# Kernel tuning notes

Measured on AMD Instinct MI355X. Metric: run time of the kernel, lower is better.

Reference implementation:

```python
import jax, jax.numpy as jnp
import numpy as np

NUM_HEADS = 16


def setup_inputs() -> dict:
    key = jax.random.key(0)
    k1, k2, k3, k4 = jax.random.split(key, 4)
    in_dim, out_dim = 1024, 1024
    x = jax.random.normal(k1, (4, 2048, in_dim), dtype=jnp.float32)
    # nn.Linear weights stored as [out, in]; we keep that convention.
    s = 1.0 / np.sqrt(in_dim)
    Wq = jax.random.uniform(k2, (out_dim, in_dim), jnp.float32, -s, s)
    Wk = jax.random.uniform(k3, (out_dim, in_dim), jnp.float32, -s, s)
    Wv = jax.random.uniform(k4, (out_dim, in_dim), jnp.float32, -s, s)
    return {"x": x, "Wq": Wq, "Wk": Wk, "Wv": Wv}


def reference(x, Wq, Wk, Wv):
    b, n, _ = x.shape
    out_dim = Wq.shape[0]
    h = NUM_HEADS
    d = out_dim // h  # head_dim

    def split_heads(t):  # [b,n,out] -> [b,h,n,d]
        return t.reshape(b, n, h, d).transpose(0, 2, 1, 3)

    q = split_heads(x @ Wq.T)
    k = split_heads(x @ Wk.T)
    v = split_heads(x @ Wv.T)

    scores = jnp.einsum("bhqd,bhkd->bhqk", q, k) / jnp.sqrt(jnp.float32(d))
    causal = jnp.tril(jnp.ones((n, n), dtype=bool))
    scores = jnp.where(causal, scores, -jnp.inf)
    attn = jax.nn.softmax(scores, axis=-1)
    out = jnp.einsum("bhqk,bhkd->bhqd", attn, v)
    return out.transpose(0, 2, 1, 3).reshape(b, n, out_dim)
```

## Files before the change

### kernel.cpp

```cpp
#include <hip/hip_runtime.h>

typedef __attribute__((ext_vector_type(8))) short short8;
typedef __attribute__((ext_vector_type(4))) short short4v;
typedef __attribute__((ext_vector_type(4))) float floatx4;
typedef __attribute__((ext_vector_type(16))) float floatx16;
typedef __attribute__((ext_vector_type(2))) int iv2;

#define GLOBAL_AS __attribute__((address_space(1)))
#define LDS_AS __attribute__((address_space(3)))

__device__ __forceinline__ short f2bs(float f) {
    union { float f; unsigned u; } v; v.f = f;
    unsigned r = v.u + 0x7fffu + ((v.u >> 16) & 1u);
    return (short)(r >> 16);
}

#if __has_builtin(__builtin_amdgcn_cvt_pk_bf16_f32)
typedef __attribute__((ext_vector_type(2))) __bf16 bf16x2;
__device__ __forceinline__ unsigned pk2(float a, float b) {
    union { bf16x2 v; unsigned u; } u;
    u.v = __builtin_amdgcn_cvt_pk_bf16_f32(a, b);
    return u.u;
}
#else
__device__ __forceinline__ unsigned pk2(float a, float b) {
    union { float f; unsigned u; } x, y; x.f = a; y.f = b;
    return ((y.u + 0x8000u) & 0xffff0000u) | ((x.u + 0x8000u) >> 16);
}
#endif

__global__ __launch_bounds__(256) void cast_all(const float* __restrict__ x,
                                                const float* __restrict__ Wq,
                                                const float* __restrict__ Wk,
                                                const float* __restrict__ Wv,
                                                short* __restrict__ xb,
                                                short* __restrict__ wb) {
    int b = blockIdx.x;
    int t = threadIdx.x;
    const float* src;
    short* dst;
    int idx;
    if (b < 8192) {
        src = x; dst = xb; idx = b * 1024 + t * 4;
    } else {
        int r = b - 8192;
        int wz = r >> 10;
        src = (wz == 0) ? Wq : (wz == 1) ? Wk : Wv;
        dst = wb + wz * (1 << 20);
        idx = (r & 1023) * 1024 + t * 4;
    }
    float4 v = *(const float4*)(src + idx);
    short4v o;
    o.x = f2bs(v.x); o.y = f2bs(v.y); o.z = f2bs(v.z); o.w = f2bs(v.w);
    *(short4v*)(dst + idx) = o;
}

__global__ __launch_bounds__(256) void qkv_gemm(const short* __restrict__ xb,
                                                const short* __restrict__ wb,
                                                short* __restrict__ qout,
                                                short* __restrict__ kout,
                                                short* __restrict__ vtout) {
    __shared__ short As[2][128 * 64];
    __shared__ short Bs[2][128 * 64];
    const int K = 1024;
    int tid = threadIdx.x;
    int lane = tid & 63;
    int wid = tid >> 6;
    int quad = lane >> 4;
    int l16 = lane & 15;
    int wm = (wid >> 1) * 64;
    int wn = (wid & 1) * 64;
    int bm = blockIdx.x * 128;
    int bn = blockIdx.y * 128;
    const short* W = wb + (size_t)blockIdx.z * K * 1024;

    floatx4 acc[4][4];
#pragma unroll
    for (int i = 0; i < 4; i++)
#pragma unroll
        for (int j = 0; j < 4; j++) acc[i][j] = (floatx4){0.f, 0.f, 0.f, 0.f};

    int srow = tid >> 3;
    int ssw = ((tid & 7) ^ (srow & 7)) * 8;

#define STAGE_AB(cb, kk) do { \
    _Pragma("unroll") for (int l = 0; l < 4; l++) { \
        const short* g = xb + (size_t)(bm + srow + l * 32) * K + (kk) + ssw; \
        __builtin_amdgcn_global_load_lds((const GLOBAL_AS void*)g, \
            (LDS_AS void*)(&As[cb][0] + tid * 8 + l * 2048), 16, 0, 0); \
    } \
    _Pragma("unroll") for (int l = 0; l < 4; l++) { \
        const short* g = W + (size_t)(bn + srow + l * 32) * K + (kk) + ssw; \
        __builtin_amdgcn_global_load_lds((const GLOBAL_AS void*)g, \
            (LDS_AS void*)(&Bs[cb][0] + tid * 8 + l * 2048), 16, 0, 0); \
    } \
} while (0)

    STAGE_AB(0, 0);

    for (int T = 0; T < 16; T++) {
        int cur = T & 1;
        __builtin_amdgcn_sched_barrier(0);
        __builtin_amdgcn_s_barrier();
        __builtin_amdgcn_sched_barrier(0);
        if (T < 15) {
            STAGE_AB(cur ^ 1, (T + 1) * 64);
            asm volatile("s_waitcnt vmcnt(8)" ::: "memory");
        } else {
            asm volatile("s_waitcnt vmcnt(0)" ::: "memory");
        }
        __builtin_amdgcn_sched_barrier(0);
        __builtin_amdgcn_s_barrier();
        __builtin_amdgcn_sched_barrier(0);

        const short* Ac = &As[cur][0];
        const short* Bc = &Bs[cur][0];
#pragma unroll
        for (int s = 0; s < 2; s++) {
            int slot = ((s * 4 + quad) ^ (l16 & 7)) * 8;
            short8 af[4], bf[4];
#pragma unroll
            for (int i = 0; i < 4; i++)
                af[i] = *(const short8*)(Ac + (wm + i * 16 + l16) * 64 + slot);
#pragma unroll
            for (int j = 0; j < 4; j++)
                bf[j] = *(const short8*)(Bc + (wn + j * 16 + l16) * 64 + slot);
#pragma unroll
            for (int i = 0; i < 4; i++)
#pragma unroll
                for (int j = 0; j < 4; j++)
                    acc[i][j] = __builtin_amdgcn_mfma_f32_16x16x32_bf16(af[i], bf[j], acc[i][j], 0, 0, 0);
        }
    }
#undef STAGE_AB

    if (blockIdx.z == 2) {
#pragma unroll
        for (int i = 0; i < 4; i++) {
#pragma unroll
            for (int j = 0; j < 4; j++) {
                int m = bm + wm + i * 16 + quad * 4;
                int c = bn + wn + j * 16 + l16;
                int b = m >> 11, nn = m & 2047, h = c >> 6, dd = c & 63;
                short4v pk;
                pk.x = f2bs(acc[i][j][0]);
                pk.y = f2bs(acc[i][j][1]);
                pk.z = f2bs(acc[i][j][2]);
                pk.w = f2bs(acc[i][j][3]);
                *(short4v*)(vtout + ((size_t)(b * 16 + h) * 64 + dd) * 2048 + nn) = pk;
            }
        }
    } else {
        short* dst = (blockIdx.z == 0) ? qout : kout;
        float qs = (blockIdx.z == 0) ? 0.180336881f : 1.0f;
#pragma unroll
        for (int i = 0; i < 4; i++) {
#pragma unroll
            for (int j = 0; j < 4; j++) {
#pragma unroll
                for (int r = 0; r < 4; r++) {
                    int m = bm + wm + i * 16 + quad * 4 + r;
                    int c = bn + wn + j * 16 + l16;
                    dst[((size_t)((m >> 11) * 16 + (c >> 6)) * 2048 + (m & 2047)) * 64 + (c & 63)] =
                        f2bs(acc[i][j][r] * qs);
                }
            }
        }
    }
}

__global__ __launch_bounds__(256, 2) void attn(const short* __restrict__ q,
                                               const short* __restrict__ k,
                                               const short* __restrict__ vt,
                                               float* __restrict__ out) {
    __shared__ short Ks[4][64 * 64];
    __shared__ short Vs[4][64 * 64];

    int tid = threadIdx.x;
    int lane = tid & 63;
    int wid = tid >> 6;
    int l32 = lane & 31;
    int half = lane >> 5;

    int flat = blockIdx.x;
    int xcd = flat & 7;
    int slot = flat >> 3;
    int bh = xcd * 8 + (slot >> 3);
    int qx = slot & 7;
    int b = bh >> 4, h = bh & 15;

    const short* qp = q + (size_t)(b * 16 + h) * 2048 * 64;
    const short* kp = k + (size_t)(b * 16 + h) * 2048 * 64;
    const short* vp = vt + (size_t)(b * 16 + h) * 64 * 2048;

    int srow = tid >> 3;
    int ssw = ((tid & 7) ^ (srow & 7)) * 8;

#define BARRIER() asm volatile("s_barrier" ::: "memory")
#define STAGE_KV(cb, kvb) do { \
    _Pragma("unroll") for (int l = 0; l < 2; l++) { \
        const short* g = kp + (size_t)((kvb) + srow + l * 32) * 64 + ssw; \
        __builtin_amdgcn_global_load_lds((const GLOBAL_AS void*)g, \
            (LDS_AS void*)(&Ks[cb][0] + tid * 8 + l * 2048), 16, 0, 0); \
    } \
    _Pragma("unroll") for (int l = 0; l < 2; l++) { \
        const short* g = vp + (size_t)(srow + l * 32) * 2048 + (kvb) + ssw; \
        __builtin_amdgcn_global_load_lds((const GLOBAL_AS void*)g, \
            (LDS_AS void*)(&Vs[cb][0] + tid * 8 + l * 2048), 16, 0, 0); \
    } \
} while (0)

#define STREAM_TILE(qf, qlane, oacc, rs, isdiag) do { \
    floatx16 sacc[2]; \
    _Pragma("unroll") for (int kb = 0; kb < 2; kb++) \
    _Pragma("unroll") for (int e = 0; e < 16; e++) sacc[kb][e] = 0.f; \
    __builtin_amdgcn_s_setprio(1); \
    _Pragma("unroll") for (int s = 0; s < 4; s++) { \
        _Pragma("unroll") for (int kb = 0; kb < 2; kb++) { \
            int key = kb * 32 + l32; \
            int c = s * 2 + half; \
            short8 kf = *(const short8*)(Kc + key * 64 + ((c ^ (key & 7)) * 8)); \
            sacc[kb] = __builtin_amdgcn_mfma_f32_32x32x16_bf16(kf, qf[s], sacc[kb], 0, 0, 0); \
        } \
    } \
    __builtin_amdgcn_s_setprio(0); \
    unsigned W0[2][4], W1[2][4]; \
    _Pragma("unroll") for (int kb = 0; kb < 2; kb++) { \
        _Pragma("unroll") for (int e = 0; e < 16; e++) { \
            float p = __builtin_amdgcn_exp2f(sacc[kb][e]); \
            if (isdiag) { \
                int key = kvb + kb * 32 + (e & 3) + 8 * (e >> 2) + 4 * half; \
                p = (key > (qlane)) ? 0.f : p; \
            } \
            sacc[kb][e] = p; \
            rs += p; \
        } \
        _Pragma("unroll") for (int g = 0; g < 4; g++) { \
            W0[kb][g] = pk2(sacc[kb][4 * g + 0], sacc[kb][4 * g + 1]); \
            W1[kb][g] = pk2(sacc[kb][4 * g + 2], sacc[kb][4 * g + 3]); \
        } \
    } \
    __builtin_amdgcn_s_setprio(1); \
    _Pragma("unroll") for (int s = 0; s < 4; s++) { \
        int kb = s >> 1; \
        int g0 = (s & 1) * 2; \
        int g1 = g0 + 1; \
        iv2 r0 = __builtin_amdgcn_permlane32_swap(W0[kb][g0], W0[kb][g1], false, false); \
        iv2 r1 = __builtin_amdgcn_permlane32_swap(W1[kb][g0], W1[kb][g1], false, false); \
        union { int4 v; short8 s8; } pu; \
        pu.v.x = r0.x; pu.v.y = r1.x; pu.v.z = r0.y; pu.v.w = r1.y; \
        short8 pf = pu.s8; \
        _Pragma("unroll") for (int nt = 0; nt < 2; nt++) { \
            int d = nt * 32 + l32; \
            int c = s * 2 + half; \
            short8 vf = *(const short8*)(Vc + d * 64 + ((c ^ (d & 7)) * 8)); \
            oacc[nt] = __builtin_amdgcn_mfma_f32_32x32x16_bf16(pf, vf, oacc[nt], 0, 0, 0); \
        } \
    } \
    __builtin_amdgcn_s_setprio(0); \
} while (0)

#define EPILOG(rs, oacc, qrow_w) do { \
    float tot = (rs) + __shfl_xor((rs), 32); \
    float inv = 1.0f / tot; \
    float invr[16]; \
    _Pragma("unroll") for (int e = 0; e < 16; e++) \
        invr[e] = __shfl(inv, (e & 3) + 8 * (e >> 2) + 4 * half); \
    _Pragma("unroll") for (int nt = 0; nt < 2; nt++) { \
        _Pragma("unroll") for (int e = 0; e < 16; e++) { \
            int r = (e & 3) + 8 * (e >> 2) + 4 * half; \
            int nn = (qrow_w) + r; \
            out[((size_t)b * 2048 + nn) * 1024 + h * 64 + nt * 32 + l32] = oacc[nt][e] * invr[e]; \
        } \
    } \
} while (0)

    int qA = qx;
    int qB = 15 - qx;
    int NT = 2 * qB + 2;
    int lastA = 2 * qA + 1;

    int qrowA = qA * 128 + wid * 32;
    int qrowB = qB * 128 + wid * 32;
    int qlaneA = qrowA + l32;
    int qlaneB = qrowB + l32;

    short8 qfA[4], qfB[4];
#pragma unroll
    for (int s = 0; s < 4; s++) {
        qfA[s] = *(const short8*)(qp + (size_t)qlaneA * 64 + s * 16 + half * 8);
        qfB[s] = *(const short8*)(qp + (size_t)qlaneB * 64 + s * 16 + half * 8);
    }

    floatx16 oaccA[2], oaccB[2];
#pragma unroll
    for (int nt = 0; nt < 2; nt++)
#pragma unroll
        for (int e = 0; e < 16; e++) { oaccA[nt][e] = 0.f; oaccB[nt][e] = 0.f; }
    float rsA = 0.f, rsB = 0.f;

    STAGE_KV(0, 0);
    STAGE_KV(1, 64);

    for (int t = 0; t < NT; t++) {
        int kvb = t * 64;

        if (t + 1 < NT) {
            asm volatile("s_waitcnt vmcnt(4)" ::: "memory");
        } else {
            asm volatile("s_waitcnt vmcnt(0)" ::: "memory");
        }
        BARRIER();

        if (t + 2 < NT) STAGE_KV((t + 2) & 3, kvb + 128);

        const short* Kc = &Ks[t & 3][0];
        const short* Vc = &Vs[t & 3][0];

        if (t <= lastA) {
            bool dA = (kvb + 63 > qrowA);
            STREAM_TILE(qfA, qlaneA, oaccA, rsA, dA);
        }
        {
            bool dB = (kvb + 63 > qrowB);
            STREAM_TILE(qfB, qlaneB, oaccB, rsB, dB);
        }
    }

    EPILOG(rsA, oaccA, qrowA);
    EPILOG(rsB, oaccB, qrowB);

#undef STREAM_TILE
#undef EPILOG
#undef STAGE_KV
#undef BARRIER
}

extern "C" void kernel_launch(void* const* d_in, const int* in_sizes, int n_in,
                              void* d_out, int out_size, void* d_ws, size_t ws_size,
                              hipStream_t stream) {
    const float* x = (const float*)d_in[0];
    const float* Wq = (const float*)d_in[1];
    const float* Wk = (const float*)d_in[2];
    const float* Wv = (const float*)d_in[3];
    float* out = (float*)d_out;
    char* ws = (char*)d_ws;

    short* xb = (short*)ws;
    short* wb = (short*)(ws + (16u << 20));
    short* qb = (short*)(ws + (22u << 20));
    short* kb = (short*)(ws + (38u << 20));
    short* vtb = (short*)(ws + (54u << 20));

    cast_all<<<8192 + 3 * 1024, 256, 0, stream>>>(x, Wq, Wk, Wv, xb, wb);
    qkv_gemm<<<dim3(64, 8, 3), 256, 0, stream>>>(xb, wb, qb, kb, vtb);
    attn<<<512, 256, 0, stream>>>(qb, kb, vtb, out);
}
```

Before: 213.0 us.

## Split paired causal q-tiles into one tile per block with heaviest-first ordering

The attention kernel stops pairing a light and a heavy causal query tile in each block. Each block now handles a single 128-row query tile, and the grid doubles to 1024 blocks, ordered so the longest tiles launch first. KV staging drops from a 4-deep to a 2-deep LDS ring, and launch bounds are raised to allow 4 blocks per CU for higher occupancy. In exchange, K/V tiles are no longer shared across two query tiles, so global and LDS traffic per output rises. The shallower prefetch also adds an extra barrier per iteration and leaves less latency hiding.

```diff
diff --git a/kernel.cpp b/kernel.cpp
--- a/kernel.cpp
+++ b/kernel.cpp
@@ -169,12 +169,12 @@
     }
 }
 
-__global__ __launch_bounds__(256, 2) void attn(const short* __restrict__ q,
+__global__ __launch_bounds__(256, 4) void attn(const short* __restrict__ q,
                                                const short* __restrict__ k,
                                                const short* __restrict__ vt,
                                                float* __restrict__ out) {
-    __shared__ short Ks[4][64 * 64];
-    __shared__ short Vs[4][64 * 64];
+    __shared__ short Ks[2][64 * 64];
+    __shared__ short Vs[2][64 * 64];
 
     int tid = threadIdx.x;
     int lane = tid & 63;
@@ -183,10 +183,8 @@
     int half = lane >> 5;
 
     int flat = blockIdx.x;
-    int xcd = flat & 7;
-    int slot = flat >> 3;
-    int bh = xcd * 8 + (slot >> 3);
-    int qx = slot & 7;
+    int qt = 15 - (flat >> 6);
+    int bh = flat & 63;
     int b = bh >> 4, h = bh & 15;
 
     const short* qp = q + (size_t)(b * 16 + h) * 2048 * 64;
@@ -275,60 +273,44 @@
     } \
 } while (0)
 
-    int qA = qx;
-    int qB = 15 - qx;
-    int NT = 2 * qB + 2;
-    int lastA = 2 * qA + 1;
-
-    int qrowA = qA * 128 + wid * 32;
-    int qrowB = qB * 128 + wid * 32;
-    int qlaneA = qrowA + l32;
-    int qlaneB = qrowB + l32;
-
-    short8 qfA[4], qfB[4];
-#pragma unroll
-    for (int s = 0; s < 4; s++) {
-        qfA[s] = *(const short8*)(qp + (size_t)qlaneA * 64 + s * 16 + half * 8);
-        qfB[s] = *(const short8*)(qp + (size_t)qlaneB * 64 + s * 16 + half * 8);
-    }
-
-    floatx16 oaccA[2], oaccB[2];
+    int NT = 2 * qt + 2;
+    int qrow = qt * 128 + wid * 32;
+    int qlane = qrow + l32;
+
+    short8 qf[4];
+#pragma unroll
+    for (int s = 0; s < 4; s++)
+        qf[s] = *(const short8*)(qp + (size_t)qlane * 64 + s * 16 + half * 8);
+
+    floatx16 oacc[2];
 #pragma unroll
     for (int nt = 0; nt < 2; nt++)
 #pragma unroll
-        for (int e = 0; e < 16; e++) { oaccA[nt][e] = 0.f; oaccB[nt][e] = 0.f; }
-    float rsA = 0.f, rsB = 0.f;
+        for (int e = 0; e < 16; e++) oacc[nt][e] = 0.f;
+    float rs = 0.f;
 
     STAGE_KV(0, 0);
-    STAGE_KV(1, 64);
 
     for (int t = 0; t < NT; t++) {
         int kvb = t * 64;
 
+        BARRIER();
         if (t + 1 < NT) {
+            STAGE_KV((t + 1) & 1, kvb + 64);
             asm volatile("s_waitcnt vmcnt(4)" ::: "memory");
         } else {
             asm volatile("s_waitcnt vmcnt(0)" ::: "memory");
         }
         BARRIER();
 
-        if (t + 2 < NT) STAGE_KV((t + 2) & 3, kvb + 128);
-
-        const short* Kc = &Ks[t & 3][0];
-        const short* Vc = &Vs[t & 3][0];
-
-        if (t <= lastA) {
-            bool dA = (kvb + 63 > qrowA);
-            STREAM_TILE(qfA, qlaneA, oaccA, rsA, dA);
-        }
-        {
-            bool dB = (kvb + 63 > qrowB);
-            STREAM_TILE(qfB, qlaneB, oaccB, rsB, dB);
-        }
+        const short* Kc = &Ks[t & 1][0];
+        const short* Vc = &Vs[t & 1][0];
+
+        bool d = (kvb + 63 > qrow);
+        STREAM_TILE(qf, qlane, oacc, rs, d);
     }
 
-    EPILOG(rsA, oaccA, qrowA);
-    EPILOG(rsB, oaccB, qrowB);
+    EPILOG(rs, oacc, qrow);
 
 #undef STREAM_TILE
 #undef EPILOG
@@ -354,5 +336,5 @@
 
     cast_all<<<8192 + 3 * 1024, 256, 0, stream>>>(x, Wq, Wk, Wv, xb, wb);
     qkv_gemm<<<dim3(64, 8, 3), 256, 0, stream>>>(xb, wb, qb, kb, vtb);
-    attn<<<512, 256, 0, stream>>>(qb, kb, vtb, out);
-}
+    attn<<<1024, 256, 0, stream>>>(qb, kb, vtb, out);
+}
```

New measurement: 210.6 us. No clear change (-1.1%).
